# Performance work log

Measured on AMD Instinct MI355X. Metric: run time of the kernel, lower is better.

Reference implementation:

```python
import jax, jax.numpy as jnp
import numpy as np
from jax import lax

START, STOP = 10, 11
NEG = -10000.0
B, T, E, HD, K, V = 64, 512, 512, 1024, 12, 50000
H = HD // 2


def setup_inputs() -> dict:
    key = jax.random.key(0)
    ks = jax.random.split(key, 20)
    sentence = jax.random.randint(ks[0], (B, T), 1, V)
    seq_lens = jnp.sort(jax.random.randint(ks[1], (B,), 1, T + 1))[::-1]
    embed = jax.random.normal(ks[2], (V, E), jnp.float32) * 0.1
    embed = embed.at[0].set(0.0)  # padding_idx=0
    s = 0.05
    Wi_f = jax.random.normal(ks[3], (4 * H, E), jnp.float32) * s
    Wh_f = jax.random.normal(ks[4], (4 * H, H), jnp.float32) * s
    b_f = jax.random.normal(ks[5], (4 * H,), jnp.float32) * s
    Wi_b = jax.random.normal(ks[6], (4 * H, E), jnp.float32) * s
    Wh_b = jax.random.normal(ks[7], (4 * H, H), jnp.float32) * s
    b_b = jax.random.normal(ks[8], (4 * H,), jnp.float32) * s
    h0 = jax.random.normal(ks[9], (2, B, H), jnp.float32)
    c0 = jax.random.normal(ks[10], (2, B, H), jnp.float32)
    W_out = jax.random.normal(ks[11], (K, HD), jnp.float32) * s
    b_out = jax.random.normal(ks[12], (K,), jnp.float32) * s
    transitions = jax.random.normal(ks[13], (K, K), jnp.float32)
    transitions = transitions.at[START, :].set(NEG).at[:, STOP].set(NEG)
    return dict(sentence=sentence, seq_lens=seq_lens, embed=embed,
                Wi_f=Wi_f, Wh_f=Wh_f, b_f=b_f, Wi_b=Wi_b, Wh_b=Wh_b, b_b=b_b,
                h0=h0, c0=c0, W_out=W_out, b_out=b_out, transitions=transitions)


def _lstm(x, h0, c0, Wi, Wh, b):
    # x: [B,T,E] -> outputs [B,T,H]; torch gate order i,f,g,o
    def step(carry, x_t):
        h, c = carry
        g = x_t @ Wi.T + h @ Wh.T + b
        i, f, gg, o = jnp.split(g, 4, axis=-1)
        c = jax.nn.sigmoid(f) * c + jax.nn.sigmoid(i) * jnp.tanh(gg)
        h = jax.nn.sigmoid(o) * jnp.tanh(c)
        return (h, c), h
    _, out = lax.scan(step, (h0, c0), x.transpose(1, 0, 2))
    return out.transpose(1, 0, 2)


def _features(sentence, seq_lens, embed, Wi_f, Wh_f, b_f, Wi_b, Wh_b, b_b, h0, c0, W_out, b_out):
    mask = jnp.arange(T)[None, :] < seq_lens[:, None]  # [B,T]
    emb = embed[sentence] * mask[:, :, None]
    out_f = _lstm(emb, h0[0], c0[0], Wi_f, Wh_f, b_f)
    # backward direction == packed reversal within each sequence length
    rev_idx = jnp.clip(seq_lens[:, None] - 1 - jnp.arange(T)[None, :], 0, T - 1)
    rev_emb = jnp.take_along_axis(emb, rev_idx[:, :, None], axis=1) * mask[:, :, None]
    out_b_rev = _lstm(rev_emb, h0[1], c0[1], Wi_b, Wh_b, b_b)
    out_b = jnp.take_along_axis(out_b_rev, rev_idx[:, :, None], axis=1)
    out = jnp.concatenate([out_f, out_b], axis=-1) * mask[:, :, None]
    feats = out @ W_out.T + b_out  # [B,T,K]
    return feats, mask


def _viterbi(feats, mask, transitions):
    fv0 = jnp.full((B, K), NEG, feats.dtype).at[:, START].set(0.0)
    ident = jnp.arange(K, dtype=jnp.int32)[None, :]

    def step(fv, inp):
        feat_t, m_t = inp  # [B,K], [B]
        sc = fv[:, None, :] + transitions[None, :, :]  # [B,next,prev]
        bp = jnp.argmax(sc, axis=2).astype(jnp.int32)
        val = jnp.max(sc, axis=2) + feat_t
        fv_new = jnp.where(m_t[:, None], val, fv)
        bp = jnp.where(m_t[:, None], bp, ident)
        return fv_new, bp

    fv, bps = lax.scan(step, fv0, (feats.transpose(1, 0, 2), mask.T))
    term = fv + transitions[STOP][None, :]
    scores = jnp.max(term, axis=-1)
    best = jnp.argmax(term, axis=-1).astype(jnp.int32)

    def back(tag, bp_t):
        prev = jnp.take_along_axis(bp_t, tag[:, None], axis=1)[:, 0]
        return prev, tag

    _, tags = lax.scan(back, best, bps, reverse=True)  # [T,B]
    return scores, tags.T  # valid predictions are preds[b, :seq_lens[b]]


def reference(sentence, seq_lens, embed, Wi_f, Wh_f, b_f, Wi_b, Wh_b, b_b, h0, c0, W_out, b_out, transitions):
    embed = embed.at[0].set(0.0)
    feats, mask = _features(sentence, seq_lens, embed, Wi_f, Wh_f, b_f, Wi_b, Wh_b, b_b, h0, c0, W_out, b_out)
    scores, preds = _viterbi(feats, mask, transitions)
    return scores, preds
```

## Files before the change

### kernel.cpp

```cpp
#include <hip/hip_runtime.h>
#include <stdint.h>

#define BSZ 64
#define TSEQ 512
#define KTAG 12
#define START_TAG 10
#define STOP_TAG 11

#define TPH 64
#define NPH 8
#define NWG 256
#define BLK 256

#define FIX_SCALE 4294967296.0
#define FIX_INV 2.3283064365386963e-10

typedef unsigned long long u64t;

#define BAR_BYTES 4096
#define FEATS_OFF BAR_BYTES
#define FEATS_BYTES (BSZ * TSEQ * KTAG * 8)
#define HBUF_OFF (FEATS_OFF + FEATS_BYTES)
#define HBUF_BYTES (2 * 512 * 128 * 4)
#define CBUF_OFF (HBUF_OFF + HBUF_BYTES)
#define CBUF_BYTES (NWG * 256 * 4)
#define BPS_OFF (CBUF_OFF + CBUF_BYTES)
#define BPS_BYTES (TSEQ * BSZ * KTAG)
#define XP_OFF (BPS_OFF + BPS_BYTES)
#define XP_BYTES (64 * 4 * TPH * 32 * 32 * 4)
#define XP2_OFF (XP_OFF + XP_BYTES)
#define XP2_BYTES XP_BYTES

#define LW_OFF 0
#define LH_OFF 16384
#define LG_OFF 32768
#define LXP_OFF 36864
#define LHL_OFF 37920
#define LCS_OFF 38176
#define LBI_OFF 38432
#define LWO_OFF 38464
#define LSL_OFF 38560
#define LMX_OFF 38592
#define LSTM_SMEM_FLOATS 38596
#define LSTM_SMEM_BYTES (LSTM_SMEM_FLOATS * 4)

#define PW_OFF 0
#define PE_OFF 8192
#define PT_OFF 16384
#define PRE_SMEM_FLOATS 16448
#define PRE_SMEM_BYTES (PRE_SMEM_FLOATS * 4)

__device__ __forceinline__ float sigm(float x) { return 1.f / (1.f + expf(-x)); }

__global__ void init_state(const float* __restrict__ h0, const float* __restrict__ c0,
                           float* __restrict__ hbuf, float* __restrict__ cbuf) {
  int i = blockIdx.x * 256 + threadIdx.x;
  if (i < 65536) {
    int u = i >> 7, ch = i & 127;
    int ct = ch >> 5, c = ch & 31;
    int dir = ct >> 1, b = ((ct & 1) << 5) + c;
    hbuf[i] = h0[(dir * 64 + b) * 512 + u];
  } else {
    int j = i - 65536;
    int wg = j >> 8, r = j & 255;
    int ct = wg >> 6, ut = wg & 63;
    int uu = r >> 5, c = r & 31;
    int dir = ct >> 1, b = ((ct & 1) << 5) + c;
    cbuf[j] = c0[(dir * 64 + b) * 512 + ut * 8 + uu];
  }
}

__global__ __launch_bounds__(256, 2) void pre_gemm(
    int phase, const int* __restrict__ sentence, const int* __restrict__ seq_lens,
    const float* __restrict__ embed, const float* __restrict__ Wi_f,
    const float* __restrict__ Wi_b, float* __restrict__ xp, float* __restrict__ xp2) {
  extern __shared__ float sm[];
  float* wiS = sm + PW_OFF;
  float* embS = sm + PE_OFF;
  int* tokS = (int*)(sm + PT_OFF);

  const int tid = threadIdx.x;
  const int bx = blockIdx.x;
  const int kh = bx >> 7;
  const int dirut = bx & 127;
  const int dir = dirut >> 6, ut = dirut & 63;
  const int yo = blockIdx.y;
  const int t0 = phase * TPH;
  if (t0 >= seq_lens[yo * 8]) return;
  const int u0 = ut * 8;
  const int e0 = kh * 256;
  const float* Wi = dir ? Wi_b : Wi_f;
  float* dst = kh ? xp2 : xp;

  for (int j = 0; j < 32; ++j) {
    int row = (j >> 3) * 512 + u0 + (j & 7);
    int ee = tid;
    wiS[ee * 32 + ((((j >> 2) ^ (ee & 7)) << 2) | (j & 3))] = Wi[row * 512 + e0 + ee];
  }

  const int lane = tid & 63, w = tid >> 6;
  const int es = lane >> 3, tl8 = lane & 7;
  const int tile = w * 8 + tl8;
  const int jt = tile & 3, rt = tile >> 2;
  const int rr = tid & 63, seg = tid >> 6;
  const int rq = rr >> 2, rl = rr & 3;
  const float* wp0b = wiS + (((jt * 2) ^ es) << 2) + es * 32;
  const float* wp1b = wiS + (((jt * 2 + 1) ^ es) << 2) + es * 32;
  const float* ep0 = embS + es * 64 + (((rt * 2) ^ es) << 2);
  const float* ep1 = embS + es * 64 + (((rt * 2 + 1) ^ es) << 2);
  const bool hi1 = (lane & 8) != 0;
  const bool hi2 = (lane & 16) != 0;
  const bool hi3 = (lane & 32) != 0;
  const int ab1 = hi1 ? 4 : 0, bb = hi2 ? 4 : 0, ab2 = hi3 ? 2 : 0;

  for (int ib = 0; ib < 8; ++ib) {
    const int b = yo * 8 + ib;
    const int sl = seq_lens[b];
    if (t0 >= sl) break;
    const int ct = dir * 2 + (b >> 5);
    const int cc = b & 31;

    __syncthreads();
    if (tid < 64) {
      int tg = t0 + tid;
      int pos = dir ? (sl - 1 - tg) : tg;
      pos = min(max(pos, 0), 511);
      tokS[tid] = sentence[b * 512 + pos];
    }
    __syncthreads();

    const int mytok = tokS[rr];
    float4 vb[2][8];
    {
      const float* src = embed + (size_t)mytok * 512 + e0 + seg * 32;
#pragma unroll
      for (int q = 0; q < 8; ++q) vb[0][q] = *(const float4*)(src + q * 4);
    }
    float acc[8][8];
#pragma unroll
    for (int a = 0; a < 8; ++a)
#pragma unroll
      for (int b2 = 0; b2 < 8; ++b2) acc[a][b2] = 0.f;

#pragma unroll
    for (int kk = 0; kk < 2; ++kk) {
      if (kk) __syncthreads();
#pragma unroll
      for (int q = 0; q < 8; ++q) {
        const int el = seg * 32 + q * 4;
        const float4 v = vb[kk & 1][q];
        embS[(el + 0) * 64 + (((rq ^ ((el + 0) & 7)) << 2) | rl)] = v.x;
        embS[(el + 1) * 64 + (((rq ^ ((el + 1) & 7)) << 2) | rl)] = v.y;
        embS[(el + 2) * 64 + (((rq ^ ((el + 2) & 7)) << 2) | rl)] = v.z;
        embS[(el + 3) * 64 + (((rq ^ ((el + 3) & 7)) << 2) | rl)] = v.w;
      }
      if (kk < 1) {
        const float* src = embed + (size_t)mytok * 512 + e0 + 128 + seg * 32;
#pragma unroll
        for (int q = 0; q < 8; ++q) vb[(kk + 1) & 1][q] = *(const float4*)(src + q * 4);
      }
      __syncthreads();
      const float* wp0 = wp0b + kk * 128 * 32;
      const float* wp1 = wp1b + kk * 128 * 32;
#pragma unroll
      for (int i = 0; i < 16; ++i) {
        const float4 w0 = *(const float4*)(wp0 + i * 256);
        const float4 w1 = *(const float4*)(wp1 + i * 256);
        const float4 x0 = *(const float4*)(ep0 + i * 512);
        const float4 x1 = *(const float4*)(ep1 + i * 512);
        float wv[8] = {w0.x, w0.y, w0.z, w0.w, w1.x, w1.y, w1.z, w1.w};
        float xv[8] = {x0.x, x0.y, x0.z, x0.w, x1.x, x1.y, x1.z, x1.w};
#pragma unroll
        for (int a = 0; a < 8; ++a)
#pragma unroll
          for (int b2 = 0; b2 < 8; ++b2) acc[a][b2] = fmaf(wv[a], xv[b2], acc[a][b2]);
      }
    }

    float r1[4][8];
#pragma unroll
    for (int a = 0; a < 4; ++a)
#pragma unroll
      for (int b2 = 0; b2 < 8; ++b2) {
        float sendv = hi1 ? acc[a][b2] : acc[a + 4][b2];
        float keepv = hi1 ? acc[a + 4][b2] : acc[a][b2];
        r1[a][b2] = keepv + __shfl_xor(sendv, 8, 64);
      }
    float r2[4][4];
#pragma unroll
    for (int a = 0; a < 4; ++a)
#pragma unroll
      for (int b2 = 0; b2 < 4; ++b2) {
        float sendv = hi2 ? r1[a][b2] : r1[a][b2 + 4];
        float keepv = hi2 ? r1[a][b2 + 4] : r1[a][b2];
        r2[a][b2] = keepv + __shfl_xor(sendv, 16, 64);
      }
    float r3[2][4];
#pragma unroll
    for (int a = 0; a < 2; ++a)
#pragma unroll
      for (int b2 = 0; b2 < 4; ++b2) {
        float sendv = hi3 ? r2[a][b2] : r2[a + 2][b2];
        float keepv = hi3 ? r2[a + 2][b2] : r2[a][b2];
        r3[a][b2] = keepv + __shfl_xor(sendv, 32, 64);
      }
    const size_t base = (size_t)(ut * 4 + ct) * (TPH * 1024) + (size_t)cc * 32;
#pragma unroll
    for (int a = 0; a < 2; ++a)
#pragma unroll
      for (int b2 = 0; b2 < 4; ++b2) {
        int tau = rt * 8 + bb + b2;
        if (t0 + tau < sl)
          dst[base + (size_t)tau * 1024 + (jt * 8 + ab1 + ab2 + a)] = r3[a][b2];
      }
  }
}

__global__ __launch_bounds__(BLK, 1) void lstm_phase(
    int phase, const int* __restrict__ seq_lens, const float* __restrict__ Wh_f,
    const float* __restrict__ Wh_b, const float* __restrict__ b_f,
    const float* __restrict__ b_b, const float* __restrict__ W_out,
    const float* __restrict__ xp, const float* __restrict__ xp2,
    float* __restrict__ hbuf, float* __restrict__ cbuf,
    unsigned long long* __restrict__ featsFix, unsigned* __restrict__ bar) {
  extern __shared__ float sm[];
  float* wS = sm + LW_OFF;
  float* hS = sm + LH_OFF;
  float* gS = sm + LG_OFF;
  float* xpS = sm + LXP_OFF;
  float* hlS = sm + LHL_OFF;
  float* cstS = sm + LCS_OFF;
  float* biasS = sm + LBI_OFF;
  float* woutS = sm + LWO_OFF;
  int* slS = (int*)(sm + LSL_OFF);
  int* mslS = (int*)(sm + LMX_OFF);

  const int tid = threadIdx.x;
  const int bid = blockIdx.x;
  const int ut = bid & 63, ct = bid >> 6;
  const int u0 = ut * 8, ch0 = ct * 32, dir = ct >> 1;
  const float* Wh = dir ? Wh_b : Wh_f;
  const float* bb = dir ? b_b : b_f;

  if (tid < 32) slS[tid] = seq_lens[((ct & 1) << 5) + tid];
  __syncthreads();
  if (tid == 0) {
    int m = 0;
    for (int c = 0; c < 32; ++c) m = max(m, slS[c]);
    *mslS = m;
  }
  __syncthreads();
  const int gmax = *mslS;
  const int t0 = phase * TPH;
  if (t0 >= gmax) return;

  for (int j = 0; j < 32; ++j) {
    int row = (j >> 3) * 512 + u0 + (j & 7);
    for (int ee = tid; ee < 512; ee += BLK)
      wS[ee * 32 + ((((j >> 2) ^ (ee & 7)) << 2) | (j & 3))] = Wh[row * 512 + ee];
  }
  if (tid < 96) woutS[tid] = W_out[(tid >> 3) * 1024 + dir * 512 + u0 + (tid & 7)];
  if (tid < 32) biasS[tid] = bb[(tid >> 3) * 512 + u0 + (tid & 7)];
  cstS[tid] = cbuf[bid * 256 + tid];
  __syncthreads();

  const int lane = tid & 63, w = tid >> 6;
  const int tp = lane & 15, jt = tp & 3, ct2 = tp >> 2;
  const int es = w * 4 + (lane >> 4);
  const int esw = es & 7;
  const int nst = min(TPH, gmax - t0);

  const float* wpA = wS + es * 32 + (((jt * 2) ^ esw) << 2);
  const float* wpB = wS + es * 32 + (((jt * 2 + 1) ^ esw) << 2);
  const float* hpA = hS + es * 32 + (((ct2 * 2) ^ esw) << 2);
  const float* hpB = hS + es * 32 + (((ct2 * 2 + 1) ^ esw) << 2);

  const size_t xb0 = (size_t)(ut * 4 + ct) * TPH * 1024;
  float4 xr = *(const float4*)(xp + xb0 + tid * 4);
  float4 xr2 = *(const float4*)(xp2 + xb0 + tid * 4);

  for (int tl = 0; tl < nst; ++tl) {
    const int t = t0 + tl;
    const float* hcur = hbuf + (t & 1) * 65536;
    float* hnxt = hbuf + ((t + 1) & 1) * 65536;

    if (tid == 0) {
      while (__hip_atomic_load(&bar[ct * 64], __ATOMIC_RELAXED,
                               __HIP_MEMORY_SCOPE_AGENT) < (unsigned)t) {}
    }
    __syncthreads();

    {
      u64t hq[32];
#pragma unroll
      for (int it = 0; it < 16; ++it) {
        int u = it * 32 + (tid >> 3), q = tid & 7;
        const u64t* p = (const u64t*)(hcur + u * 128 + ch0 + q * 4);
        hq[2 * it] = __hip_atomic_load(p, __ATOMIC_RELAXED, __HIP_MEMORY_SCOPE_AGENT);
        hq[2 * it + 1] =
            __hip_atomic_load(p + 1, __ATOMIC_RELAXED, __HIP_MEMORY_SCOPE_AGENT);
      }
#pragma unroll
      for (int it = 0; it < 16; ++it) {
        int u = it * 32 + (tid >> 3), q = tid & 7;
        union { u64t q2[2]; float4 v; } uu2;
        uu2.q2[0] = hq[2 * it];
        uu2.q2[1] = hq[2 * it + 1];
        *(float4*)(hS + u * 32 + ((q ^ (u & 7)) << 2)) = uu2.v;
      }
    }
    {
      int c = tid >> 3, j4 = tid & 7;
      float* d = xpS + c * 33 + j4 * 4;
      d[0] = xr.x + xr2.x;
      d[1] = xr.y + xr2.y;
      d[2] = xr.z + xr2.z;
      d[3] = xr.w + xr2.w;
    }
    if (tl + 1 < nst) {
      xr = *(const float4*)(xp + xb0 + (size_t)(tl + 1) * 1024 + tid * 4);
      xr2 = *(const float4*)(xp2 + xb0 + (size_t)(tl + 1) * 1024 + tid * 4);
    }
    __syncthreads();

    float acc[8][8];
#pragma unroll
    for (int a = 0; a < 8; ++a)
#pragma unroll
      for (int b2 = 0; b2 < 8; ++b2) acc[a][b2] = 0.f;
    for (int io = 0; io < 4; ++io) {
#pragma unroll
      for (int ii = 0; ii < 8; ++ii) {
        const int off = (io * 8 + ii) * 512;
        const float4 w0 = *(const float4*)(wpA + off);
        const float4 w1 = *(const float4*)(wpB + off);
        const float4 x0 = *(const float4*)(hpA + off);
        const float4 x1 = *(const float4*)(hpB + off);
        float wv[8] = {w0.x, w0.y, w0.z, w0.w, w1.x, w1.y, w1.z, w1.w};
        float xv[8] = {x0.x, x0.y, x0.z, x0.w, x1.x, x1.y, x1.z, x1.w};
#pragma unroll
        for (int a = 0; a < 8; ++a)
#pragma unroll
          for (int b2 = 0; b2 < 8; ++b2) acc[a][b2] = fmaf(wv[a], xv[b2], acc[a][b2]);
      }
    }

    const bool hi1 = (lane & 16) != 0;
    float r1[4][8];
#pragma unroll
    for (int a = 0; a < 4; ++a)
#pragma unroll
      for (int b2 = 0; b2 < 8; ++b2) {
        float sendv = hi1 ? acc[a][b2] : acc[a + 4][b2];
        float keepv = hi1 ? acc[a + 4][b2] : acc[a][b2];
        r1[a][b2] = keepv + __shfl_xor(sendv, 16, 64);
      }
    const bool hi2 = (lane & 32) != 0;
    float r2[4][4];
#pragma unroll
    for (int a = 0; a < 4; ++a)
#pragma unroll
      for (int b2 = 0; b2 < 4; ++b2) {
        float sendv = hi2 ? r1[a][b2] : r1[a][b2 + 4];
        float keepv = hi2 ? r1[a][b2 + 4] : r1[a][b2];
        r2[a][b2] = keepv + __shfl_xor(sendv, 32, 64);
      }
    const int ab = hi1 ? 4 : 0, bbs = hi2 ? 4 : 0;
#pragma unroll
    for (int a = 0; a < 4; ++a) {
      float4 v = make_float4(r2[a][0], r2[a][1], r2[a][2], r2[a][3]);
      *(float4*)(gS + w * 1024 + (jt * 8 + ab + a) * 32 + ct2 * 8 + bbs) = v;
    }
    __syncthreads();

    {
      const int uu = tid >> 5, c = tid & 31;
      const int slc = slS[c];
      float s0 = 0.f, s1 = 0.f, s2 = 0.f, s3 = 0.f;
#pragma unroll
      for (int w2 = 0; w2 < 4; ++w2) {
        const float* gp = gS + w2 * 1024 + uu * 32 + c;
        s0 += gp[0];
        s1 += gp[256];
        s2 += gp[512];
        s3 += gp[768];
      }
      const bool xvalid = (t < slc);
      float x0 = xvalid ? xpS[c * 33 + uu] : 0.f;
      float x1 = xvalid ? xpS[c * 33 + 8 + uu] : 0.f;
      float x2 = xvalid ? xpS[c * 33 + 16 + uu] : 0.f;
      float x3 = xvalid ? xpS[c * 33 + 24 + uu] : 0.f;
      float iv = s0 + x0 + biasS[uu];
      float fv = s1 + x1 + biasS[8 + uu];
      float gv = s2 + x2 + biasS[16 + uu];
      float ov = s3 + x3 + biasS[24 + uu];
      float cn = sigm(fv) * cstS[uu * 32 + c] + sigm(iv) * tanhf(gv);
      float hn = sigm(ov) * tanhf(cn);
      cstS[uu * 32 + c] = cn;
      __hip_atomic_store(&hnxt[(u0 + uu) * 128 + ch0 + c], hn, __ATOMIC_RELAXED,
                         __HIP_MEMORY_SCOPE_AGENT);
      hlS[uu * 32 + c] = hn;
    }
    asm volatile("s_waitcnt vmcnt(0)" ::: "memory");
    __syncthreads();

    if (tid == 0) {
      unsigned o = __hip_atomic_fetch_add(&bar[ct * 64 + 16], 1u, __ATOMIC_RELAXED,
                                          __HIP_MEMORY_SCOPE_AGENT);
      if (o == (unsigned)(t + 1) * 64u - 1u)
        __hip_atomic_store(&bar[ct * 64], (unsigned)(t + 1), __ATOMIC_RELAXED,
                           __HIP_MEMORY_SCOPE_AGENT);
    }

    for (int base = 0; base < 384; base += 256) {
      int idx = base + tid;
      if (idx < 384) {
        int c = idx / 12, k = idx % 12;
        int sl = slS[c];
        if (t < sl) {
          float pacc = 0.f;
#pragma unroll
          for (int uu = 0; uu < 8; ++uu) pacc += hlS[uu * 32 + c] * woutS[k * 8 + uu];
          int tt = dir ? (sl - 1 - t) : t;
          double y = (double)pacc * FIX_SCALE;
          long long q = (long long)(y + (y >= 0.0 ? 0.5 : -0.5));
          atomicAdd(&featsFix[((size_t)(((ct & 1) << 5) + c) * 512 + tt) * 12 + k],
                    (unsigned long long)q);
        }
      }
    }
  }
  cbuf[bid * 256 + tid] = cstS[tid];
}

__global__ __launch_bounds__(64) void viterbi2(
    const int* __restrict__ seq_lens, const float* __restrict__ b_out,
    const float* __restrict__ transitions,
    const unsigned long long* __restrict__ featsFix,
    unsigned char* __restrict__ bps, float* __restrict__ out) {
  __shared__ unsigned char tagB[512];
  const int b = blockIdx.x;
  const int lane = threadIdx.x;
  const int k = lane < 12 ? lane : 0;
  const int sl = seq_lens[b];
  float trow[12];
#pragma unroll
  for (int p = 0; p < 12; ++p) trow[p] = transitions[k * 12 + p];
  const float bo = b_out[k];
  float fvv[12];
#pragma unroll
  for (int p = 0; p < 12; ++p) fvv[p] = (p == START_TAG) ? 0.f : -10000.f;
  const unsigned long long* fbase = featsFix + (size_t)b * 512 * 12;
  long long fx = (long long)fbase[k];
  for (int t = 0; t < TSEQ; ++t) {
    float best = fvv[0] + trow[0];
    int arg = 0;
#pragma unroll
    for (int p = 1; p < 12; ++p) {
      float v = fvv[p] + trow[p];
      if (v > best) { best = v; arg = p; }
    }
    float feat = (float)((double)fx * FIX_INV) + bo;
    if (t + 1 < TSEQ) fx = (long long)fbase[(t + 1) * 12 + k];
    const bool m = t < sl;
    float nv = m ? (best + feat) : fvv[k];
    int bpv = m ? arg : k;
    if (lane < 12) bps[((size_t)t * 64 + b) * 12 + lane] = (unsigned char)bpv;
#pragma unroll
    for (int p = 0; p < 12; ++p) fvv[p] = __shfl(nv, p, 64);
  }
  __syncthreads();
  if (lane == 0) {
    float best = fvv[0] + transitions[STOP_TAG * 12 + 0];
    int arg = 0;
    for (int kk = 1; kk < 12; ++kk) {
      float v = fvv[kk] + transitions[STOP_TAG * 12 + kk];
      if (v > best) { best = v; arg = kk; }
    }
    out[b] = best;
    int tag = arg;
    const uint32_t* rowp = (const uint32_t*)bps;
    uint32_t r0, r1, r2;
    {
      size_t off = ((size_t)511 * 64 + b) * 3;
      r0 = rowp[off]; r1 = rowp[off + 1]; r2 = rowp[off + 2];
    }
    for (int t = 511; t >= 0; --t) {
      uint32_t n0 = 0, n1 = 0, n2 = 0;
      if (t > 0) {
        size_t off = ((size_t)(t - 1) * 64 + b) * 3;
        n0 = rowp[off]; n1 = rowp[off + 1]; n2 = rowp[off + 2];
      }
      tagB[t] = (unsigned char)tag;
      uint32_t sel = (tag < 4) ? (r0 >> (tag * 8))
                   : (tag < 8) ? (r1 >> ((tag - 4) * 8))
                               : (r2 >> ((tag - 8) * 8));
      tag = (int)(sel & 0xffu);
      r0 = n0; r1 = n1; r2 = n2;
    }
  }
  __syncthreads();
  for (int t = lane; t < 512; t += 64) out[64 + (size_t)b * 512 + t] = (float)tagB[t];
}

extern "C" void kernel_launch(void* const* d_in, const int* in_sizes, int n_in,
                              void* d_out, int out_size, void* d_ws, size_t ws_size,
                              hipStream_t stream) {
  (void)in_sizes; (void)n_in; (void)out_size; (void)ws_size;
  const int* sentence = (const int*)d_in[0];
  const int* seq_lens = (const int*)d_in[1];
  const float* embed = (const float*)d_in[2];
  const float* Wi_f = (const float*)d_in[3];
  const float* Wh_f = (const float*)d_in[4];
  const float* b_f = (const float*)d_in[5];
  const float* Wi_b = (const float*)d_in[6];
  const float* Wh_b = (const float*)d_in[7];
  const float* b_b = (const float*)d_in[8];
  const float* h0 = (const float*)d_in[9];
  const float* c0 = (const float*)d_in[10];
  const float* W_out = (const float*)d_in[11];
  const float* b_out = (const float*)d_in[12];
  const float* trans = (const float*)d_in[13];

  char* ws = (char*)d_ws;
  unsigned* bar = (unsigned*)ws;
  unsigned long long* featsFix = (unsigned long long*)(ws + FEATS_OFF);
  float* hbuf = (float*)(ws + HBUF_OFF);
  float* cbuf = (float*)(ws + CBUF_OFF);
  unsigned char* bps = (unsigned char*)(ws + BPS_OFF);
  float* xpw = (float*)(ws + XP_OFF);
  float* xpw2 = (float*)(ws + XP2_OFF);

  hipMemsetAsync(d_ws, 0, FEATS_OFF + FEATS_BYTES, stream);

  hipFuncSetAttribute((const void*)lstm_phase,
                      hipFuncAttributeMaxDynamicSharedMemorySize, LSTM_SMEM_BYTES);
  hipFuncSetAttribute((const void*)pre_gemm,
                      hipFuncAttributeMaxDynamicSharedMemorySize, PRE_SMEM_BYTES);

  init_state<<<dim3(512), dim3(256), 0, stream>>>(h0, c0, hbuf, cbuf);

  for (int p = 0; p < NPH; ++p) {
    pre_gemm<<<dim3(256, 8), dim3(BLK), PRE_SMEM_BYTES, stream>>>(
        p, sentence, seq_lens, embed, Wi_f, Wi_b, xpw, xpw2);
    int pv = p;
    void* kargs[] = {(void*)&pv,   (void*)&seq_lens, (void*)&Wh_f,  (void*)&Wh_b,
                     (void*)&b_f,  (void*)&b_b,      (void*)&W_out, (void*)&xpw,
                     (void*)&xpw2, (void*)&hbuf,     (void*)&cbuf,  (void*)&featsFix,
                     (void*)&bar};
    hipLaunchCooperativeKernel((const void*)lstm_phase, dim3(NWG), dim3(BLK), kargs,
                               LSTM_SMEM_BYTES, stream);
  }
  viterbi2<<<dim3(64), dim3(64), 0, stream>>>(seq_lens, b_out, trans, featsFix, bps,
                                              (float*)d_out);
}
```

Measured before the change: 6.129 ms.

## Use split-bf16 MFMA for LSTM recurrent matmul with transposed h layout

Replaces the scalar FP32 FMA recurrent GEMM in the persistent LSTM kernel with bf16 MFMA 16x16x32 instructions, using a hi/lo bf16 split of weights and hidden state (three products) to approximate FP32 accuracy. The hidden-state buffer and cell-state layouts are transposed to channel-major so each workgroup loads contiguous rows, and the shared-memory layout is rebuilt with XOR swizzles. The goal is to cut the ALU-bound per-step matmul latency on the serial recurrence. It raises LDS use to about 157KB and adds per-step bf16 conversion work, and it adds a small precision risk from dropping the lo*lo term.

```diff
diff --git a/kernel.cpp b/kernel.cpp
--- a/kernel.cpp
+++ b/kernel.cpp
@@ -16,12 +16,14 @@
 #define FIX_INV 2.3283064365386963e-10
 
 typedef unsigned long long u64t;
+typedef __attribute__((ext_vector_type(8))) short bf16x8;
+typedef __attribute__((ext_vector_type(4))) float f32x4;
 
 #define BAR_BYTES 4096
 #define FEATS_OFF BAR_BYTES
 #define FEATS_BYTES (BSZ * TSEQ * KTAG * 8)
 #define HBUF_OFF (FEATS_OFF + FEATS_BYTES)
-#define HBUF_BYTES (2 * 512 * 128 * 4)
+#define HBUF_BYTES (2 * 128 * 512 * 4)
 #define CBUF_OFF (HBUF_OFF + HBUF_BYTES)
 #define CBUF_BYTES (NWG * 256 * 4)
 #define BPS_OFF (CBUF_OFF + CBUF_BYTES)
@@ -31,18 +33,19 @@
 #define XP2_OFF (XP_OFF + XP_BYTES)
 #define XP2_BYTES XP_BYTES
 
-#define LW_OFF 0
-#define LH_OFF 16384
-#define LG_OFF 32768
-#define LXP_OFF 36864
-#define LHL_OFF 37920
-#define LCS_OFF 38176
-#define LBI_OFF 38432
-#define LWO_OFF 38464
-#define LSL_OFF 38560
-#define LMX_OFF 38592
-#define LSTM_SMEM_FLOATS 38596
-#define LSTM_SMEM_BYTES (LSTM_SMEM_FLOATS * 4)
+#define WAH_OFF 0
+#define WAL_OFF 32768
+#define HBH_OFF 65536
+#define HBL_OFF 98304
+#define GS_OFF 131072
+#define XPS_OFF 149504
+#define HLS_OFF 154112
+#define CST_OFF 155136
+#define BIAS_OFF 156160
+#define WOUT_OFF 156288
+#define SL_OFF 156672
+#define MSL_OFF 156800
+#define LSTM_SMEM_BYTES 156804
 
 #define PW_OFF 0
 #define PE_OFF 8192
@@ -52,11 +55,23 @@
 
 __device__ __forceinline__ float sigm(float x) { return 1.f / (1.f + expf(-x)); }
 
+__device__ __forceinline__ unsigned cvtpk(float a, float b) {
+  unsigned r;
+  asm("v_cvt_pk_bf16_f32 %0, %1, %2" : "=v"(r) : "v"(a), "v"(b));
+  return r;
+}
+__device__ __forceinline__ void split2(float a, float b, unsigned& hi, unsigned& lo) {
+  hi = cvtpk(a, b);
+  float ha = __uint_as_float(hi << 16);
+  float hb = __uint_as_float(hi & 0xFFFF0000u);
+  lo = cvtpk(a - ha, b - hb);
+}
+
 __global__ void init_state(const float* __restrict__ h0, const float* __restrict__ c0,
                            float* __restrict__ hbuf, float* __restrict__ cbuf) {
   int i = blockIdx.x * 256 + threadIdx.x;
   if (i < 65536) {
-    int u = i >> 7, ch = i & 127;
+    int ch = i >> 9, u = i & 511;
     int ct = ch >> 5, c = ch & 31;
     int dir = ct >> 1, b = ((ct & 1) << 5) + c;
     hbuf[i] = h0[(dir * 64 + b) * 512 + u];
@@ -64,7 +79,7 @@
     int j = i - 65536;
     int wg = j >> 8, r = j & 255;
     int ct = wg >> 6, ut = wg & 63;
-    int uu = r >> 5, c = r & 31;
+    int c = r >> 3, uu = r & 7;
     int dir = ct >> 1, b = ((ct & 1) << 5) + c;
     cbuf[j] = c0[(dir * 64 + b) * 512 + ut * 8 + uu];
   }
@@ -223,17 +238,19 @@
     const float* __restrict__ xp, const float* __restrict__ xp2,
     float* __restrict__ hbuf, float* __restrict__ cbuf,
     unsigned long long* __restrict__ featsFix, unsigned* __restrict__ bar) {
-  extern __shared__ float sm[];
-  float* wS = sm + LW_OFF;
-  float* hS = sm + LH_OFF;
-  float* gS = sm + LG_OFF;
-  float* xpS = sm + LXP_OFF;
-  float* hlS = sm + LHL_OFF;
-  float* cstS = sm + LCS_OFF;
-  float* biasS = sm + LBI_OFF;
-  float* woutS = sm + LWO_OFF;
-  int* slS = (int*)(sm + LSL_OFF);
-  int* mslS = (int*)(sm + LMX_OFF);
+  extern __shared__ char smc[];
+  char* WAH = smc + WAH_OFF;
+  char* WAL = smc + WAL_OFF;
+  char* HBH = smc + HBH_OFF;
+  char* HBL = smc + HBL_OFF;
+  float* gS = (float*)(smc + GS_OFF);
+  float* xpS = (float*)(smc + XPS_OFF);
+  float* hlS = (float*)(smc + HLS_OFF);
+  float* cstS = (float*)(smc + CST_OFF);
+  float* biasS = (float*)(smc + BIAS_OFF);
+  float* woutS = (float*)(smc + WOUT_OFF);
+  int* slS = (int*)(smc + SL_OFF);
+  int* mslS = (int*)(smc + MSL_OFF);
 
   const int tid = threadIdx.x;
   const int bid = blockIdx.x;
@@ -254,26 +271,35 @@
   const int t0 = phase * TPH;
   if (t0 >= gmax) return;
 
-  for (int j = 0; j < 32; ++j) {
-    int row = (j >> 3) * 512 + u0 + (j & 7);
-    for (int ee = tid; ee < 512; ee += BLK)
-      wS[ee * 32 + ((((j >> 2) ^ (ee & 7)) << 2) | (j & 3))] = Wh[row * 512 + ee];
+  {
+    const int jj = tid & 31, sgw = tid >> 5;
+    const int row = (jj >> 3) * 512 + u0 + (jj & 7);
+    const unsigned swz = (unsigned)((jj & 15) << 4);
+    for (int it = 0; it < 8; ++it) {
+      const int e = it * 64 + sgw * 8;
+      float4 v0 = *(const float4*)(Wh + row * 512 + e);
+      float4 v1 = *(const float4*)(Wh + row * 512 + e + 4);
+      unsigned h0, h1, h2, h3, l0, l1, l2, l3;
+      split2(v0.x, v0.y, h0, l0);
+      split2(v0.z, v0.w, h1, l1);
+      split2(v1.x, v1.y, h2, l2);
+      split2(v1.z, v1.w, h3, l3);
+      const unsigned off = (unsigned)(jj * 1024) + (((unsigned)(e * 2)) ^ swz);
+      *(uint4*)(WAH + off) = make_uint4(h0, h1, h2, h3);
+      *(uint4*)(WAL + off) = make_uint4(l0, l1, l2, l3);
+    }
   }
   if (tid < 96) woutS[tid] = W_out[(tid >> 3) * 1024 + dir * 512 + u0 + (tid & 7)];
   if (tid < 32) biasS[tid] = bb[(tid >> 3) * 512 + u0 + (tid & 7)];
   cstS[tid] = cbuf[bid * 256 + tid];
   __syncthreads();
 
-  const int lane = tid & 63, w = tid >> 6;
-  const int tp = lane & 15, jt = tp & 3, ct2 = tp >> 2;
-  const int es = w * 4 + (lane >> 4);
-  const int esw = es & 7;
+  const int l = tid & 63, w = tid >> 6;
+  const int lr = l & 15;
+  const int ef = (l >> 4) * 8;
+  const int cc = tid & 31, sg = tid >> 5;
+  const int cE = tid >> 3, uuE = tid & 7;
   const int nst = min(TPH, gmax - t0);
-
-  const float* wpA = wS + es * 32 + (((jt * 2) ^ esw) << 2);
-  const float* wpB = wS + es * 32 + (((jt * 2 + 1) ^ esw) << 2);
-  const float* hpA = hS + es * 32 + (((ct2 * 2) ^ esw) << 2);
-  const float* hpB = hS + es * 32 + (((ct2 * 2 + 1) ^ esw) << 2);
 
   const size_t xb0 = (size_t)(ut * 4 + ct) * TPH * 1024;
   float4 xr = *(const float4*)(xp + xb0 + tid * 4);
@@ -292,30 +318,36 @@
 
     {
       u64t hq[32];
-#pragma unroll
-      for (int it = 0; it < 16; ++it) {
-        int u = it * 32 + (tid >> 3), q = tid & 7;
-        const u64t* p = (const u64t*)(hcur + u * 128 + ch0 + q * 4);
-        hq[2 * it] = __hip_atomic_load(p, __ATOMIC_RELAXED, __HIP_MEMORY_SCOPE_AGENT);
-        hq[2 * it + 1] =
-            __hip_atomic_load(p + 1, __ATOMIC_RELAXED, __HIP_MEMORY_SCOPE_AGENT);
-      }
-#pragma unroll
-      for (int it = 0; it < 16; ++it) {
-        int u = it * 32 + (tid >> 3), q = tid & 7;
-        union { u64t q2[2]; float4 v; } uu2;
-        uu2.q2[0] = hq[2 * it];
-        uu2.q2[1] = hq[2 * it + 1];
-        *(float4*)(hS + u * 32 + ((q ^ (u & 7)) << 2)) = uu2.v;
-      }
-    }
-    {
-      int c = tid >> 3, j4 = tid & 7;
-      float* d = xpS + c * 33 + j4 * 4;
-      d[0] = xr.x + xr2.x;
-      d[1] = xr.y + xr2.y;
-      d[2] = xr.z + xr2.z;
-      d[3] = xr.w + xr2.w;
+      const u64t* hrow = (const u64t*)(hcur + (ch0 + cc) * 512);
+#pragma unroll
+      for (int it = 0; it < 8; ++it) {
+        const u64t* p = hrow + ((it * 64 + sg * 8) >> 1);
+        hq[4 * it + 0] = __hip_atomic_load(p + 0, __ATOMIC_RELAXED, __HIP_MEMORY_SCOPE_AGENT);
+        hq[4 * it + 1] = __hip_atomic_load(p + 1, __ATOMIC_RELAXED, __HIP_MEMORY_SCOPE_AGENT);
+        hq[4 * it + 2] = __hip_atomic_load(p + 2, __ATOMIC_RELAXED, __HIP_MEMORY_SCOPE_AGENT);
+        hq[4 * it + 3] = __hip_atomic_load(p + 3, __ATOMIC_RELAXED, __HIP_MEMORY_SCOPE_AGENT);
+      }
+      const unsigned swz = (unsigned)((cc & 15) << 4);
+#pragma unroll
+      for (int it = 0; it < 8; ++it) {
+        const int e = it * 64 + sg * 8;
+        unsigned hw[4], lw[4];
+#pragma unroll
+        for (int p2 = 0; p2 < 4; ++p2) {
+          u64t q2 = hq[4 * it + p2];
+          float fa = __uint_as_float((unsigned)(q2 & 0xFFFFFFFFu));
+          float fb = __uint_as_float((unsigned)(q2 >> 32));
+          split2(fa, fb, hw[p2], lw[p2]);
+        }
+        const unsigned off = (unsigned)(cc * 1024) + (((unsigned)(e * 2)) ^ swz);
+        *(uint4*)(HBH + off) = make_uint4(hw[0], hw[1], hw[2], hw[3]);
+        *(uint4*)(HBL + off) = make_uint4(lw[0], lw[1], lw[2], lw[3]);
+      }
+    }
+    {
+      float* d = xpS + cE * 36 + uuE * 4;
+      d[0] = xr.x + xr2.x; d[1] = xr.y + xr2.y;
+      d[2] = xr.z + xr2.z; d[3] = xr.w + xr2.w;
     }
     if (tl + 1 < nst) {
       xr = *(const float4*)(xp + xb0 + (size_t)(tl + 1) * 1024 + tid * 4);
@@ -323,83 +355,75 @@
     }
     __syncthreads();
 
-    float acc[8][8];
-#pragma unroll
-    for (int a = 0; a < 8; ++a)
-#pragma unroll
-      for (int b2 = 0; b2 < 8; ++b2) acc[a][b2] = 0.f;
-    for (int io = 0; io < 4; ++io) {
-#pragma unroll
-      for (int ii = 0; ii < 8; ++ii) {
-        const int off = (io * 8 + ii) * 512;
-        const float4 w0 = *(const float4*)(wpA + off);
-        const float4 w1 = *(const float4*)(wpB + off);
-        const float4 x0 = *(const float4*)(hpA + off);
-        const float4 x1 = *(const float4*)(hpB + off);
-        float wv[8] = {w0.x, w0.y, w0.z, w0.w, w1.x, w1.y, w1.z, w1.w};
-        float xv[8] = {x0.x, x0.y, x0.z, x0.w, x1.x, x1.y, x1.z, x1.w};
-#pragma unroll
-        for (int a = 0; a < 8; ++a)
-#pragma unroll
-          for (int b2 = 0; b2 < 8; ++b2) acc[a][b2] = fmaf(wv[a], xv[b2], acc[a][b2]);
-      }
-    }
-
-    const bool hi1 = (lane & 16) != 0;
-    float r1[4][8];
-#pragma unroll
-    for (int a = 0; a < 4; ++a)
-#pragma unroll
-      for (int b2 = 0; b2 < 8; ++b2) {
-        float sendv = hi1 ? acc[a][b2] : acc[a + 4][b2];
-        float keepv = hi1 ? acc[a + 4][b2] : acc[a][b2];
-        r1[a][b2] = keepv + __shfl_xor(sendv, 16, 64);
-      }
-    const bool hi2 = (lane & 32) != 0;
-    float r2[4][4];
-#pragma unroll
-    for (int a = 0; a < 4; ++a)
-#pragma unroll
-      for (int b2 = 0; b2 < 4; ++b2) {
-        float sendv = hi2 ? r1[a][b2] : r1[a][b2 + 4];
-        float keepv = hi2 ? r1[a][b2 + 4] : r1[a][b2];
-        r2[a][b2] = keepv + __shfl_xor(sendv, 32, 64);
-      }
-    const int ab = hi1 ? 4 : 0, bbs = hi2 ? 4 : 0;
-#pragma unroll
-    for (int a = 0; a < 4; ++a) {
-      float4 v = make_float4(r2[a][0], r2[a][1], r2[a][2], r2[a][3]);
-      *(float4*)(gS + w * 1024 + (jt * 8 + ab + a) * 32 + ct2 * 8 + bbs) = v;
+    f32x4 acc00 = {0.f, 0.f, 0.f, 0.f}, acc01 = acc00, acc10 = acc00, acc11 = acc00;
+    {
+      const unsigned sw = (unsigned)(lr << 4);
+      const unsigned r0 = (unsigned)(lr * 1024), r1 = (unsigned)((16 + lr) * 1024);
+#pragma unroll
+      for (int kc = 0; kc < 4; ++kc) {
+        const unsigned eb = (unsigned)((w * 128 + kc * 32 + ef) * 2) ^ sw;
+        bf16x8 a0h = *(const bf16x8*)(WAH + r0 + eb);
+        bf16x8 a1h = *(const bf16x8*)(WAH + r1 + eb);
+        bf16x8 a0l = *(const bf16x8*)(WAL + r0 + eb);
+        bf16x8 a1l = *(const bf16x8*)(WAL + r1 + eb);
+        bf16x8 b0h = *(const bf16x8*)(HBH + r0 + eb);
+        bf16x8 b1h = *(const bf16x8*)(HBH + r1 + eb);
+        bf16x8 b0l = *(const bf16x8*)(HBL + r0 + eb);
+        bf16x8 b1l = *(const bf16x8*)(HBL + r1 + eb);
+        acc00 = __builtin_amdgcn_mfma_f32_16x16x32_bf16(a0h, b0h, acc00, 0, 0, 0);
+        acc01 = __builtin_amdgcn_mfma_f32_16x16x32_bf16(a0h, b1h, acc01, 0, 0, 0);
+        acc10 = __builtin_amdgcn_mfma_f32_16x16x32_bf16(a1h, b0h, acc10, 0, 0, 0);
+        acc11 = __builtin_amdgcn_mfma_f32_16x16x32_bf16(a1h, b1h, acc11, 0, 0, 0);
+        acc00 = __builtin_amdgcn_mfma_f32_16x16x32_bf16(a0h, b0l, acc00, 0, 0, 0);
+        acc01 = __builtin_amdgcn_mfma_f32_16x16x32_bf16(a0h, b1l, acc01, 0, 0, 0);
+        acc10 = __builtin_amdgcn_mfma_f32_16x16x32_bf16(a1h, b0l, acc10, 0, 0, 0);
+        acc11 = __builtin_amdgcn_mfma_f32_16x16x32_bf16(a1h, b1l, acc11, 0, 0, 0);
+        acc00 = __builtin_amdgcn_mfma_f32_16x16x32_bf16(a0l, b0h, acc00, 0, 0, 0);
+        acc01 = __builtin_amdgcn_mfma_f32_16x16x32_bf16(a0l, b1h, acc01, 0, 0, 0);
+        acc10 = __builtin_amdgcn_mfma_f32_16x16x32_bf16(a1l, b0h, acc10, 0, 0, 0);
+        acc11 = __builtin_amdgcn_mfma_f32_16x16x32_bf16(a1l, b1h, acc11, 0, 0, 0);
+      }
+    }
+    {
+      float* gw = gS + w * (32 * 36);
+      const int gr = (l >> 4) * 4;
+#pragma unroll
+      for (int rg = 0; rg < 4; ++rg) {
+        gw[(gr + rg) * 36 + lr] = acc00[rg];
+        gw[(gr + rg) * 36 + 16 + lr] = acc01[rg];
+        gw[(16 + gr + rg) * 36 + lr] = acc10[rg];
+        gw[(16 + gr + rg) * 36 + 16 + lr] = acc11[rg];
+      }
     }
     __syncthreads();
 
     {
-      const int uu = tid >> 5, c = tid & 31;
+      const int c = cE, uu = uuE;
       const int slc = slS[c];
       float s0 = 0.f, s1 = 0.f, s2 = 0.f, s3 = 0.f;
 #pragma unroll
       for (int w2 = 0; w2 < 4; ++w2) {
-        const float* gp = gS + w2 * 1024 + uu * 32 + c;
+        const float* gp = gS + w2 * (32 * 36) + uu * 36 + c;
         s0 += gp[0];
-        s1 += gp[256];
-        s2 += gp[512];
-        s3 += gp[768];
+        s1 += gp[8 * 36];
+        s2 += gp[16 * 36];
+        s3 += gp[24 * 36];
       }
       const bool xvalid = (t < slc);
-      float x0 = xvalid ? xpS[c * 33 + uu] : 0.f;
-      float x1 = xvalid ? xpS[c * 33 + 8 + uu] : 0.f;
-      float x2 = xvalid ? xpS[c * 33 + 16 + uu] : 0.f;
-      float x3 = xvalid ? xpS[c * 33 + 24 + uu] : 0.f;
+      float x0 = xvalid ? xpS[c * 36 + uu] : 0.f;
+      float x1 = xvalid ? xpS[c * 36 + 8 + uu] : 0.f;
+      float x2 = xvalid ? xpS[c * 36 + 16 + uu] : 0.f;
+      float x3 = xvalid ? xpS[c * 36 + 24 + uu] : 0.f;
       float iv = s0 + x0 + biasS[uu];
       float fv = s1 + x1 + biasS[8 + uu];
       float gv = s2 + x2 + biasS[16 + uu];
       float ov = s3 + x3 + biasS[24 + uu];
-      float cn = sigm(fv) * cstS[uu * 32 + c] + sigm(iv) * tanhf(gv);
+      float cn = sigm(fv) * cstS[tid] + sigm(iv) * tanhf(gv);
       float hn = sigm(ov) * tanhf(cn);
-      cstS[uu * 32 + c] = cn;
-      __hip_atomic_store(&hnxt[(u0 + uu) * 128 + ch0 + c], hn, __ATOMIC_RELAXED,
+      cstS[tid] = cn;
+      __hip_atomic_store(&hnxt[(ch0 + c) * 512 + u0 + uu], hn, __ATOMIC_RELAXED,
                          __HIP_MEMORY_SCOPE_AGENT);
-      hlS[uu * 32 + c] = hn;
+      hlS[tid] = hn;
     }
     asm volatile("s_waitcnt vmcnt(0)" ::: "memory");
     __syncthreads();
@@ -420,7 +444,7 @@
         if (t < sl) {
           float pacc = 0.f;
 #pragma unroll
-          for (int uu = 0; uu < 8; ++uu) pacc += hlS[uu * 32 + c] * woutS[k * 8 + uu];
+          for (int uu = 0; uu < 8; ++uu) pacc += hlS[c * 8 + uu] * woutS[k * 8 + uu];
           int tt = dir ? (sl - 1 - t) : t;
           double y = (double)pacc * FIX_SCALE;
           long long q = (long long)(y + (y >= 0.0 ? 0.5 : -0.5));
```

Measured after the change: 5.791 ms. 1.06x faster.
